# Kernel optimization log

Hardware: AMD Instinct MI355X
Metric: run time of the kernel (lower is better)

## Reference

```python
import jax, jax.numpy as jnp
import numpy as np

B, T, HID, OUT = 32, 2048, 1024, 1024
DV = 1024
NEG_INF = jnp.float32(-jnp.inf)


def setup_inputs() -> dict:
    key = jax.random.key(0)
    ks = jax.random.split(key, 10)
    hidden = jax.random.normal(ks[0], (B, HID), dtype=jnp.float32)
    enc_key = jax.random.normal(ks[1], (B, T, OUT), dtype=jnp.float32)
    value = jax.random.normal(ks[2], (B, T, DV), dtype=jnp.float32)
    seq_lens = jnp.maximum(jax.random.randint(ks[3], (B,), 0, T), 1).astype(jnp.int32)
    # learned parameters (PyTorch Linear: y = x @ W.T + b; we store W already transposed)
    s_q = 1.0 / np.sqrt(HID)
    s_1 = 1.0 / np.sqrt(OUT)
    s_2 = 1.0 / np.sqrt(OUT // 2)
    Wq = jax.random.uniform(ks[4], (HID, OUT), minval=-s_q, maxval=s_q, dtype=jnp.float32)
    bq = jax.random.uniform(ks[5], (OUT,), minval=-s_q, maxval=s_q, dtype=jnp.float32)
    W1 = jax.random.uniform(ks[6], (OUT, OUT // 2), minval=-s_1, maxval=s_1, dtype=jnp.float32)
    b1 = jax.random.uniform(ks[7], (OUT // 2,), minval=-s_1, maxval=s_1, dtype=jnp.float32)
    W2 = jax.random.uniform(ks[8], (OUT // 2, 1), minval=-s_2, maxval=s_2, dtype=jnp.float32)
    b2 = jax.random.uniform(ks[9], (1,), minval=-s_2, maxval=s_2, dtype=jnp.float32)
    return {"hidden": hidden, "key": enc_key, "value": value, "seq_lens": seq_lens,
            "Wq": Wq, "bq": bq, "W1": W1, "b1": b1, "W2": W2, "b2": b2}


def reference(hidden, key, value, seq_lens, Wq, bq, W1, b1, W2, b2):
    # query projection: [B, OUT]
    query = hidden @ Wq + bq
    # additive Bahdanau: tanh(key + query) -> [B, T, OUT]
    h = jnp.tanh(key + query[:, None, :])
    # 2-layer score MLP (dropout p=0.2 is identity in eval mode)
    h = h @ W1 + b1                      # [B, T, OUT//2]
    scores = (h @ W2 + b2)[..., 0]       # [B, T]
    # mask positions >= seq_len with -inf, then softmax over T
    pos = jnp.arange(scores.shape[1])
    scores = jnp.where(pos[None, :] < seq_lens[:, None], scores, NEG_INF)
    attn = jax.nn.softmax(scores, axis=-1)  # [B, T]
    # context = attn @ value -> [B, DV]
    context = jnp.einsum('bt,btd->bd', attn, value)
    return (context, attn)
```

## Files before the change

kernel.cpp:

```cpp
#include <hip/hip_runtime.h>
#include <math.h>

#define BB 32
#define TT 2048
#define DD 1024
#define HF 512

#define QKS 64
#define QCH (DD / QKS)

#define CHK 32
#define NCH (TT / CHK)

#define KSC 2.88539008177792681f

#if __has_builtin(__builtin_amdgcn_exp2f)
#define EXP2F(x) __builtin_amdgcn_exp2f(x)
#else
#define EXP2F(x) exp2f(x)
#endif

__global__ void __launch_bounds__(256) prep_query_kernel(
        const float* __restrict__ hidden, const float* __restrict__ Wq,
        const float* __restrict__ W1, const float* __restrict__ b1,
        const float* __restrict__ W2, const float* __restrict__ b2,
        float* __restrict__ w, float* __restrict__ cbias,
        float* __restrict__ qpart) {
    __shared__ float smem[BB * QCH];
    int bx  = blockIdx.x;
    int tid = threadIdx.x;

    if (bx < 4) {
        int d = bx * 256 + tid;
        const float* row = W1 + (size_t)d * HF;
        float acc = 0.0f;
        #pragma unroll 8
        for (int j = 0; j < HF; j += 4) {
            float4 a = *(const float4*)(row + j);
            float4 b = *(const float4*)(W2 + j);
            acc += a.x * b.x + a.y * b.y + a.z * b.z + a.w * b.w;
        }
        w[d] = acc;
        return;
    }
    if (bx == 4) {
        __shared__ float red[256];
        float s = b1[tid] * W2[tid] + b1[tid + 256] * W2[tid + 256];
        red[tid] = s;
        __syncthreads();
        for (int off = 128; off; off >>= 1) {
            if (tid < off) red[tid] += red[tid + off];
            __syncthreads();
        }
        if (tid == 0) cbias[0] = red[0] + b2[0];
        return;
    }
    int idx = bx - 5, otile = idx & 3, ks = idx >> 2;
    int o = otile * 256 + tid, h0 = ks * QCH;
    if (tid < 128) {
        int r = tid >> 2, c4 = (tid & 3) << 2;
        *(float4*)&smem[r * QCH + c4] = *(const float4*)&hidden[(size_t)r * DD + h0 + c4];
    }
    __syncthreads();

    float wv[QCH];
    #pragma unroll
    for (int h = 0; h < QCH; ++h)
        wv[h] = Wq[(size_t)(h0 + h) * DD + o];

    float acc[BB];
    #pragma unroll
    for (int b = 0; b < BB; ++b) acc[b] = 0.0f;
    #pragma unroll
    for (int h = 0; h < QCH; ++h) {
        #pragma unroll
        for (int b = 0; b < BB; ++b)
            acc[b] = fmaf(smem[b * QCH + h], wv[h], acc[b]);
    }
    #pragma unroll
    for (int b = 0; b < BB; ++b)
        qpart[((size_t)ks * BB + b) * DD + o] = acc[b];
}

__global__ void __launch_bounds__(256) qreduce_kernel(
        const float* __restrict__ qpart, const float* __restrict__ bq,
        const float* __restrict__ w, float* __restrict__ cb,
        float* __restrict__ query) {
    __shared__ float part[256];
    int bx = blockIdx.x, tid = threadIdx.x;
    if (bx == 256) {
        float s = w[tid] + w[tid + 256] + w[tid + 512] + w[tid + 768];
        part[tid] = s;
        __syncthreads();
        for (int off = 128; off; off >>= 1) {
            if (tid < off) part[tid] += part[tid + off];
            __syncthreads();
        }
        if (tid == 0) cb[1] = cb[0] + part[0];
        return;
    }
    int e = tid & 127, g = tid >> 7;
    int i = bx * 128 + e;
    int ks0 = g * (QKS / 2);
    float a0 = 0.0f, a1 = 0.0f, a2 = 0.0f, a3 = 0.0f;
    #pragma unroll 8
    for (int k = 0; k < QKS / 2; k += 4) {
        size_t base = (size_t)(ks0 + k) * (BB * DD) + i;
        a0 += qpart[base];
        a1 += qpart[base + (size_t)(BB * DD)];
        a2 += qpart[base + 2 * (size_t)(BB * DD)];
        a3 += qpart[base + 3 * (size_t)(BB * DD)];
    }
    part[tid] = (a0 + a1) + (a2 + a3);
    __syncthreads();
    if (g == 0) query[i] = bq[i & (DD - 1)] + part[tid] + part[tid + 128];
}

__global__ void __launch_bounds__(256, 6) score_ctx_kernel(
        const float* __restrict__ key, const float* __restrict__ value,
        const float* __restrict__ query, const float* __restrict__ w,
        const float* __restrict__ cb, const int* __restrict__ seq_lens,
        float* __restrict__ escore, float* __restrict__ psum,
        float* __restrict__ partial) {
    int n    = blockIdx.x;
    int hi   = n >> 8;
    int b    = (((n & 7) ^ hi) << 2) | ((n >> 6) & 3);
    int x    = ((n >> 3) & 7) | (hi << 3);
    int len  = seq_lens[b];
    int t0   = x * CHK;
    if (t0 >= len) return;

    __shared__ float wsh[DD];
    __shared__ float qsh[DD];
    __shared__ float esm[CHK];
    int tid = threadIdx.x;
    { int i4 = tid * 4;
      float4 w4 = *(const float4*)&w[i4];
      float4 q4 = *(const float4*)&query[(size_t)b * DD + i4];
      float4 ws = {-2.0f * w4.x, -2.0f * w4.y, -2.0f * w4.z, -2.0f * w4.w};
      float4 qs = {KSC * q4.x, KSC * q4.y, KSC * q4.z, KSC * q4.w};
      *(float4*)&wsh[i4] = ws;
      *(float4*)&qsh[i4] = qs; }
    __syncthreads();

    int wave = tid >> 6, lane = tid & 63;
    float c2 = cb[1];
    const float* kb0 = key + (size_t)b * TT * DD;

    float4 kreg[2][4];
    {
        const float* kr = kb0 + (size_t)(t0 + wave) * DD;
        #pragma unroll
        for (int s = 0; s < 4; ++s)
            kreg[0][s] = *(const float4*)(kr + s * 256 + lane * 4);
    }
    #pragma unroll
    for (int j = 0; j < 8; ++j) {
        if (j < 7) {
            const float* kr = kb0 + (size_t)(t0 + (j + 1) * 4 + wave) * DD;
            #pragma unroll
            for (int s = 0; s < 4; ++s)
                kreg[(j + 1) & 1][s] = *(const float4*)(kr + s * 256 + lane * 4);
        }
        float acc = 0.0f;
        #pragma unroll
        for (int s = 0; s < 4; ++s) {
            int d = s * 256 + lane * 4;
            float4 kv = kreg[j & 1][s];
            float4 qv = *(const float4*)&qsh[d];
            float4 wv = *(const float4*)&wsh[d];
            float r0 = __builtin_amdgcn_rcpf(EXP2F(fmaf(kv.x, KSC, qv.x)) + 1.0f);
            float r1 = __builtin_amdgcn_rcpf(EXP2F(fmaf(kv.y, KSC, qv.y)) + 1.0f);
            float r2 = __builtin_amdgcn_rcpf(EXP2F(fmaf(kv.z, KSC, qv.z)) + 1.0f);
            float r3 = __builtin_amdgcn_rcpf(EXP2F(fmaf(kv.w, KSC, qv.w)) + 1.0f);
            acc = fmaf(wv.x, r0, acc);
            acc = fmaf(wv.y, r1, acc);
            acc = fmaf(wv.z, r2, acc);
            acc = fmaf(wv.w, r3, acc);
        }
        #pragma unroll
        for (int off = 32; off; off >>= 1) acc += __shfl_down(acc, off);
        if (lane == 0) {
            int t = t0 + j * 4 + wave;
            esm[j * 4 + wave] = (t < len) ? __expf(acc + c2) : 0.0f;
        }
    }
    __syncthreads();

    if (tid < CHK) escore[(size_t)b * TT + t0 + tid] = esm[tid];
    if (tid == 0) {
        float s = 0.0f;
        #pragma unroll
        for (int i = 0; i < CHK; ++i) s += esm[i];
        psum[b * NCH + x] = s;
    }

    int d4 = tid * 4;
    const float* vbase = value + (size_t)b * TT * DD + d4;
    float4 A0 = {0.0f, 0.0f, 0.0f, 0.0f};
    float4 A1 = A0, A2 = A0, A3 = A0;
    #pragma unroll 2
    for (int tt = 0; tt < CHK; tt += 4) {
        float e0 = esm[tt], e1 = esm[tt + 1], e2 = esm[tt + 2], e3 = esm[tt + 3];
        float4 v0 = *(const float4*)(vbase + (size_t)(t0 + tt    ) * DD);
        float4 v1 = *(const float4*)(vbase + (size_t)(t0 + tt + 1) * DD);
        float4 v2 = *(const float4*)(vbase + (size_t)(t0 + tt + 2) * DD);
        float4 v3 = *(const float4*)(vbase + (size_t)(t0 + tt + 3) * DD);
        A0.x = fmaf(e0, v0.x, A0.x); A0.y = fmaf(e0, v0.y, A0.y);
        A0.z = fmaf(e0, v0.z, A0.z); A0.w = fmaf(e0, v0.w, A0.w);
        A1.x = fmaf(e1, v1.x, A1.x); A1.y = fmaf(e1, v1.y, A1.y);
        A1.z = fmaf(e1, v1.z, A1.z); A1.w = fmaf(e1, v1.w, A1.w);
        A2.x = fmaf(e2, v2.x, A2.x); A2.y = fmaf(e2, v2.y, A2.y);
        A2.z = fmaf(e2, v2.z, A2.z); A2.w = fmaf(e2, v2.w, A2.w);
        A3.x = fmaf(e3, v3.x, A3.x); A3.y = fmaf(e3, v3.y, A3.y);
        A3.z = fmaf(e3, v3.z, A3.z); A3.w = fmaf(e3, v3.w, A3.w);
    }
    float4 R;
    R.x = (A0.x + A1.x) + (A2.x + A3.x);
    R.y = (A0.y + A1.y) + (A2.y + A3.y);
    R.z = (A0.z + A1.z) + (A2.z + A3.z);
    R.w = (A0.w + A1.w) + (A2.w + A3.w);
    *(float4*)&partial[((size_t)(b * NCH + x)) * DD + d4] = R;
}

__global__ void __launch_bounds__(256) finalize_kernel(
        const float* __restrict__ partial, const float* __restrict__ escore,
        const float* __restrict__ psum, const int* __restrict__ seq_lens,
        float* __restrict__ ctx, float* __restrict__ attn) {
    __shared__ float red[NCH];
    __shared__ float part[256];
    int bx = blockIdx.x, tid = threadIdx.x;
    int b  = (bx < 256) ? (bx >> 3) : ((bx - 256) >> 1);
    int len = seq_lens[b];
    int nch = (len + CHK - 1) / CHK;

    if (tid < NCH) red[tid] = (tid < nch) ? psum[b * NCH + tid] : 0.0f;
    __syncthreads();
    #pragma unroll
    for (int off = NCH / 2; off; off >>= 1) {
        if (tid < off) red[tid] += red[tid + off];
        __syncthreads();
    }
    float Sinv = 1.0f / red[0];

    if (bx < 256) {
        int e = tid & 127, g = tid >> 7;
        int d = (bx & 7) * 128 + e;
        const float* pb = partial + (size_t)b * NCH * DD + d;
        int cbeg = g * 32, cend = min(nch, cbeg + 32);
        float a0 = 0.0f, a1 = 0.0f, a2 = 0.0f, a3 = 0.0f;
        int c = cbeg;
        for (; c + 3 < cend; c += 4) {
            a0 += pb[(size_t)(c + 0) * DD];
            a1 += pb[(size_t)(c + 1) * DD];
            a2 += pb[(size_t)(c + 2) * DD];
            a3 += pb[(size_t)(c + 3) * DD];
        }
        for (; c < cend; ++c) a0 += pb[(size_t)c * DD];
        part[tid] = (a0 + a1) + (a2 + a3);
        __syncthreads();
        if (g == 0) ctx[(size_t)b * DD + d] = (part[tid] + part[tid + 128]) * Sinv;
    } else {
        int idx = (bx - 256) * 1024 + tid * 4;
        int t   = idx & (TT - 1);
        float4 e4 = *(const float4*)&escore[(size_t)b * TT + t];
        float4 o;
        o.x = (t + 0 < len) ? e4.x * Sinv : 0.0f;
        o.y = (t + 1 < len) ? e4.y * Sinv : 0.0f;
        o.z = (t + 2 < len) ? e4.z * Sinv : 0.0f;
        o.w = (t + 3 < len) ? e4.w * Sinv : 0.0f;
        *(float4*)&attn[(size_t)b * TT + t] = o;
    }
}

extern "C" void kernel_launch(void* const* d_in, const int* in_sizes, int n_in,
                              void* d_out, int out_size, void* d_ws, size_t ws_size,
                              hipStream_t stream) {
    const float* hidden   = (const float*)d_in[0];
    const float* key      = (const float*)d_in[1];
    const float* value    = (const float*)d_in[2];
    const int*   seq_lens = (const int*)  d_in[3];
    const float* Wq       = (const float*)d_in[4];
    const float* bq       = (const float*)d_in[5];
    const float* W1       = (const float*)d_in[6];
    const float* b1       = (const float*)d_in[7];
    const float* W2       = (const float*)d_in[8];
    const float* b2       = (const float*)d_in[9];

    float* out  = (float*)d_out;
    float* ctx  = out;
    float* attn = out + BB * DD;

    float* ws      = (float*)d_ws;
    float* w       = ws;
    float* cb      = ws + 1024;
    float* query   = ws + 2048;
    float* qpart   = query + BB * DD;
    float* escore  = qpart + (size_t)QKS * BB * DD;
    float* psum    = escore + BB * TT;
    float* partial = psum + BB * NCH;

    prep_query_kernel<<<dim3(5 + 4 * QKS), dim3(256), 0, stream>>>(
        hidden, Wq, W1, b1, W2, b2, w, cb, qpart);
    qreduce_kernel<<<dim3(BB * DD / 128 + 1), dim3(256), 0, stream>>>(
        qpart, bq, w, cb, query);
    score_ctx_kernel<<<dim3(BB * NCH), dim3(256), 0, stream>>>(
        key, value, query, w, cb, seq_lens, escore, psum, partial);
    finalize_kernel<<<dim3(320), dim3(256), 0, stream>>>(
        partial, escore, psum, seq_lens, ctx, attn);
}
```

Baseline: 82.15 us.

## Fuse value accumulation into score loop with per-wave context accumulators

The score_ctx kernel now loads each value row alongside its key row and accumulates e*v in per-wave registers inside the score loop, instead of a second pass after a block barrier. Wave partial context vectors are reduced through a 16KB shared buffer at the end, and the score shuffle reduction becomes a butterfly so every lane holds the score. This removes the mid-kernel barrier and the separate value phase, so value loads overlap with the transcendental work. The cost is more registers and shared memory, and the occupancy hint drops from 6 to 5 blocks.

New measurement: 125.2 us. 52.4% more time.

```diff
diff --git a/kernel.cpp b/kernel.cpp
--- a/kernel.cpp
+++ b/kernel.cpp
@@ -116,7 +116,7 @@
     if (g == 0) query[i] = bq[i & (DD - 1)] + part[tid] + part[tid + 128];
 }
 
-__global__ void __launch_bounds__(256, 6) score_ctx_kernel(
+__global__ void __launch_bounds__(256, 5) score_ctx_kernel(
         const float* __restrict__ key, const float* __restrict__ value,
         const float* __restrict__ query, const float* __restrict__ w,
         const float* __restrict__ cb, const int* __restrict__ seq_lens,
@@ -132,7 +132,8 @@
 
     __shared__ float wsh[DD];
     __shared__ float qsh[DD];
-    __shared__ float esm[CHK];
+    __shared__ float redbuf[4][DD];
+    __shared__ float esums[4];
     int tid = threadIdx.x;
     { int i4 = tid * 4;
       float4 w4 = *(const float4*)&w[i4];
@@ -143,29 +144,43 @@
       *(float4*)&qsh[i4] = qs; }
     __syncthreads();
 
-    int wave = tid >> 6, lane = tid & 63;
+    int wave = tid >> 6, lane = tid & 63, l4 = lane * 4;
     float c2 = cb[1];
-    const float* kb0 = key + (size_t)b * TT * DD;
+    const float* kb0 = key   + (size_t)b * TT * DD;
+    const float* vb0 = value + (size_t)b * TT * DD;
+
+    float4 acc[4];
+    #pragma unroll
+    for (int s = 0; s < 4; ++s) acc[s] = make_float4(0.f, 0.f, 0.f, 0.f);
+    float esum = 0.0f;
 
     float4 kreg[2][4];
     {
         const float* kr = kb0 + (size_t)(t0 + wave) * DD;
         #pragma unroll
         for (int s = 0; s < 4; ++s)
-            kreg[0][s] = *(const float4*)(kr + s * 256 + lane * 4);
-    }
+            kreg[0][s] = *(const float4*)(kr + s * 256 + l4);
+    }
+
     #pragma unroll
     for (int j = 0; j < 8; ++j) {
+        int t = t0 + j * 4 + wave;
         if (j < 7) {
-            const float* kr = kb0 + (size_t)(t0 + (j + 1) * 4 + wave) * DD;
+            const float* kr = kb0 + (size_t)(t + 4) * DD;
             #pragma unroll
             for (int s = 0; s < 4; ++s)
-                kreg[(j + 1) & 1][s] = *(const float4*)(kr + s * 256 + lane * 4);
-        }
-        float acc = 0.0f;
+                kreg[(j + 1) & 1][s] = *(const float4*)(kr + s * 256 + l4);
+        }
+        const float* vr = vb0 + (size_t)t * DD;
+        float4 v0 = *(const float4*)(vr + l4);
+        float4 v1 = *(const float4*)(vr + 256 + l4);
+        float4 v2 = *(const float4*)(vr + 512 + l4);
+        float4 v3 = *(const float4*)(vr + 768 + l4);
+
+        float sa = 0.0f;
         #pragma unroll
         for (int s = 0; s < 4; ++s) {
-            int d = s * 256 + lane * 4;
+            int d = s * 256 + l4;
             float4 kv = kreg[j & 1][s];
             float4 qv = *(const float4*)&qsh[d];
             float4 wv = *(const float4*)&wsh[d];
@@ -173,54 +188,47 @@
             float r1 = __builtin_amdgcn_rcpf(EXP2F(fmaf(kv.y, KSC, qv.y)) + 1.0f);
             float r2 = __builtin_amdgcn_rcpf(EXP2F(fmaf(kv.z, KSC, qv.z)) + 1.0f);
             float r3 = __builtin_amdgcn_rcpf(EXP2F(fmaf(kv.w, KSC, qv.w)) + 1.0f);
-            acc = fmaf(wv.x, r0, acc);
-            acc = fmaf(wv.y, r1, acc);
-            acc = fmaf(wv.z, r2, acc);
-            acc = fmaf(wv.w, r3, acc);
+            sa = fmaf(wv.x, r0, sa);
+            sa = fmaf(wv.y, r1, sa);
+            sa = fmaf(wv.z, r2, sa);
+            sa = fmaf(wv.w, r3, sa);
         }
         #pragma unroll
-        for (int off = 32; off; off >>= 1) acc += __shfl_down(acc, off);
-        if (lane == 0) {
-            int t = t0 + j * 4 + wave;
-            esm[j * 4 + wave] = (t < len) ? __expf(acc + c2) : 0.0f;
-        }
-    }
-    __syncthreads();
-
-    if (tid < CHK) escore[(size_t)b * TT + t0 + tid] = esm[tid];
-    if (tid == 0) {
-        float s = 0.0f;
-        #pragma unroll
-        for (int i = 0; i < CHK; ++i) s += esm[i];
-        psum[b * NCH + x] = s;
-    }
+        for (int m = 1; m < 64; m <<= 1) sa += __shfl_xor(sa, m);
+
+        float e = (t < len) ? __expf(sa + c2) : 0.0f;
+        esum += e;
+        if (lane == 0) escore[(size_t)b * TT + t] = e;
+
+        acc[0].x = fmaf(e, v0.x, acc[0].x); acc[0].y = fmaf(e, v0.y, acc[0].y);
+        acc[0].z = fmaf(e, v0.z, acc[0].z); acc[0].w = fmaf(e, v0.w, acc[0].w);
+        acc[1].x = fmaf(e, v1.x, acc[1].x); acc[1].y = fmaf(e, v1.y, acc[1].y);
+        acc[1].z = fmaf(e, v1.z, acc[1].z); acc[1].w = fmaf(e, v1.w, acc[1].w);
+        acc[2].x = fmaf(e, v2.x, acc[2].x); acc[2].y = fmaf(e, v2.y, acc[2].y);
+        acc[2].z = fmaf(e, v2.z, acc[2].z); acc[2].w = fmaf(e, v2.w, acc[2].w);
+        acc[3].x = fmaf(e, v3.x, acc[3].x); acc[3].y = fmaf(e, v3.y, acc[3].y);
+        acc[3].z = fmaf(e, v3.z, acc[3].z); acc[3].w = fmaf(e, v3.w, acc[3].w);
+    }
+
+    if (lane == 0) esums[wave] = esum;
+    #pragma unroll
+    for (int s = 0; s < 4; ++s)
+        *(float4*)&redbuf[wave][s * 256 + l4] = acc[s];
+    __syncthreads();
 
     int d4 = tid * 4;
-    const float* vbase = value + (size_t)b * TT * DD + d4;
-    float4 A0 = {0.0f, 0.0f, 0.0f, 0.0f};
-    float4 A1 = A0, A2 = A0, A3 = A0;
-    #pragma unroll 2
-    for (int tt = 0; tt < CHK; tt += 4) {
-        float e0 = esm[tt], e1 = esm[tt + 1], e2 = esm[tt + 2], e3 = esm[tt + 3];
-        float4 v0 = *(const float4*)(vbase + (size_t)(t0 + tt    ) * DD);
-        float4 v1 = *(const float4*)(vbase + (size_t)(t0 + tt + 1) * DD);
-        float4 v2 = *(const float4*)(vbase + (size_t)(t0 + tt + 2) * DD);
-        float4 v3 = *(const float4*)(vbase + (size_t)(t0 + tt + 3) * DD);
-        A0.x = fmaf(e0, v0.x, A0.x); A0.y = fmaf(e0, v0.y, A0.y);
-        A0.z = fmaf(e0, v0.z, A0.z); A0.w = fmaf(e0, v0.w, A0.w);
-        A1.x = fmaf(e1, v1.x, A1.x); A1.y = fmaf(e1, v1.y, A1.y);
-        A1.z = fmaf(e1, v1.z, A1.z); A1.w = fmaf(e1, v1.w, A1.w);
-        A2.x = fmaf(e2, v2.x, A2.x); A2.y = fmaf(e2, v2.y, A2.y);
-        A2.z = fmaf(e2, v2.z, A2.z); A2.w = fmaf(e2, v2.w, A2.w);
-        A3.x = fmaf(e3, v3.x, A3.x); A3.y = fmaf(e3, v3.y, A3.y);
-        A3.z = fmaf(e3, v3.z, A3.z); A3.w = fmaf(e3, v3.w, A3.w);
-    }
+    float4 r0 = *(const float4*)&redbuf[0][d4];
+    float4 r1 = *(const float4*)&redbuf[1][d4];
+    float4 r2 = *(const float4*)&redbuf[2][d4];
+    float4 r3 = *(const float4*)&redbuf[3][d4];
     float4 R;
-    R.x = (A0.x + A1.x) + (A2.x + A3.x);
-    R.y = (A0.y + A1.y) + (A2.y + A3.y);
-    R.z = (A0.z + A1.z) + (A2.z + A3.z);
-    R.w = (A0.w + A1.w) + (A2.w + A3.w);
+    R.x = (r0.x + r1.x) + (r2.x + r3.x);
+    R.y = (r0.y + r1.y) + (r2.y + r3.y);
+    R.z = (r0.z + r1.z) + (r2.z + r3.z);
+    R.w = (r0.w + r1.w) + (r2.w + r3.w);
     *(float4*)&partial[((size_t)(b * NCH + x)) * DD + d4] = R;
+    if (tid == 0)
+        psum[b * NCH + x] = (esums[0] + esums[1]) + (esums[2] + esums[3]);
 }
 
 __global__ void __launch_bounds__(256) finalize_kernel(
```
